# Kernel tuning notes

Hardware: AMD Instinct MI355X
Metric: run time of the kernel (lower is better)

The kernel has to match this reference:

```python
import jax, jax.numpy as jnp
import numpy as np

PATCH = 14

def setup_inputs() -> dict:
    key = jax.random.key(0)
    k1, k2 = jax.random.split(key)
    frames = jax.random.normal(k1, (3, 256, 224, 224), dtype=jnp.float32)
    # per-frame masked patch indices (frame mode), values in [0, num_patches)
    mask_indices = jax.random.randint(k2, (256, 128), 0, 256, dtype=jnp.int64 if jax.config.read('jax_enable_x64') else jnp.int32)
    return {"frames": frames, "mask_indices": mask_indices}

def reference(frames, mask_indices):
    # frames: [C, T, H, W], H == W; mask_indices: [T, num_masked]
    C, T, H, W = frames.shape
    sidelen = W // PATCH  # 16
    # original: h_idx = idx % sidelen (row of patch grid), w_idx = idx // sidelen (col)
    h_idx = mask_indices % sidelen  # [T, M]
    w_idx = mask_indices // sidelen  # [T, M]
    t_idx = jnp.arange(T)[:, None]  # [T, 1] broadcasts against [T, M]
    mask = jnp.ones((T, sidelen, sidelen), dtype=frames.dtype)
    mask = mask.at[t_idx, h_idx, w_idx].set(0.0)  # zero masked patches
    # expand patch-grid mask to pixel mask [T, H, W]
    mask_full = jnp.repeat(jnp.repeat(mask, PATCH, axis=1), PATCH, axis=2)
    return frames * mask_full[None, :, :, :]
```

## Files before the change

kernel.cpp:

```cpp
#include <hip/hip_runtime.h>


constexpr int T_N    = 256;
constexpr int C_N    = 3;
constexpr int H_N    = 224;
constexpr int W_N    = 224;
constexpr int SIDE   = 16;
constexpr int PATCH  = 14;
constexpr int M_N    = 128;
constexpr int F4_ROW = W_N / 4;
constexpr int F4_BAND = PATCH * F4_ROW;
constexpr int F4_PLANE = H_N * W_N / 4;

__global__ __launch_bounds__(256)
void MaskPatches_74818330296837_kernel(const float4* __restrict__ frames,
                                       const int*    __restrict__ midx,
                                       float4*       __restrict__ out)
{
    __shared__ float mrow[SIDE];

    const int bid = blockIdx.x;
    const int ph  = bid & 15;
    const int ct  = bid >> 4;
    const int t   = ct & 255;

    const int tid = threadIdx.x;

    if (tid < SIDE) mrow[tid] = 1.0f;
    __syncthreads();
    if (tid < M_N) {
        const int idx = midx[t * M_N + tid];
        if ((idx & 15) == ph) mrow[idx >> 4] = 0.0f;
    }
    __syncthreads();

    const long long base = (long long)ct * F4_PLANE + (long long)ph * F4_BAND;

    for (int i = tid; i < F4_BAND; i += 256) {
        const int col4 = i % F4_ROW;
        const int w    = col4 * 4;
        float4 v = frames[base + i];
        v.x *= mrow[(w    ) / PATCH];
        v.y *= mrow[(w + 1) / PATCH];
        v.z *= mrow[(w + 2) / PATCH];
        v.w *= mrow[(w + 3) / PATCH];
        out[base + i] = v;
    }
}

extern "C" void kernel_launch(void* const* d_in, const int* in_sizes, int n_in,
                              void* d_out, int out_size, void* d_ws, size_t ws_size,
                              hipStream_t stream) {
    const float4* frames = (const float4*)d_in[0];
    const int*    midx   = (const int*)d_in[1];
    float4*       out    = (float4*)d_out;

    const int grid = C_N * T_N * SIDE;
    MaskPatches_74818330296837_kernel<<<grid, 256, 0, stream>>>(frames, midx, out);
}
```

Measured before the change: 55.13 us.

## Process all channels per block with nontemporal loads and wave-shuffle mask bits

Each block now covers all three channels of one frame band, so the mask is built once per (t, patch-row) instead of three times. The shared-memory mask and its two __syncthreads are replaced by a per-lane bitmask combined with xor shuffles across the 64-lane wave. All twelve loads are issued up front as nontemporal loads, with nontemporal stores at the end, to raise memory-level parallelism and avoid cache pollution. The cost is higher register use and a third as many blocks.

```diff
diff --git a/kernel.cpp b/kernel.cpp
--- a/kernel.cpp
+++ b/kernel.cpp
@@ -1,60 +1,82 @@
 #include <hip/hip_runtime.h>
 
 
-constexpr int T_N    = 256;
-constexpr int C_N    = 3;
-constexpr int H_N    = 224;
-constexpr int W_N    = 224;
-constexpr int SIDE   = 16;
-constexpr int PATCH  = 14;
-constexpr int M_N    = 128;
-constexpr int F4_ROW = W_N / 4;
+typedef float f32x4 __attribute__((ext_vector_type(4)));
+
+constexpr int T_N     = 256;
+constexpr int H_N     = 224;
+constexpr int W_N     = 224;
+constexpr int SIDE    = 16;
+constexpr int PATCH   = 14;
+constexpr int M_N     = 128;
+constexpr int F4_ROW  = W_N / 4;
 constexpr int F4_BAND = PATCH * F4_ROW;
 constexpr int F4_PLANE = H_N * W_N / 4;
+constexpr long long F4_CHAN = (long long)T_N * F4_PLANE;
 
 __global__ __launch_bounds__(256)
-void MaskPatches_74818330296837_kernel(const float4* __restrict__ frames,
-                                       const int*    __restrict__ midx,
-                                       float4*       __restrict__ out)
+void MaskPatches_74818330296837_kernel(const f32x4* __restrict__ frames,
+                                       const int*   __restrict__ midx,
+                                       f32x4*       __restrict__ out)
 {
-    __shared__ float mrow[SIDE];
+    const int bid  = blockIdx.x;
+    const int ph   = bid & 15;
+    const int t    = bid >> 4;
+    const int tid  = threadIdx.x;
+    const int lane = tid & 63;
 
-    const int bid = blockIdx.x;
-    const int ph  = bid & 15;
-    const int ct  = bid >> 4;
-    const int t   = ct & 255;
+    const int* row = midx + t * M_N;
+    const int i0 = row[lane];
+    const int i1 = row[lane + 64];
 
-    const int tid = threadIdx.x;
+    const long long base0 = (long long)t * F4_PLANE + (long long)ph * F4_BAND;
+    const bool tail = tid < (F4_BAND - 3 * 256);
+    f32x4 v[3][4];
+    #pragma unroll
+    for (int c = 0; c < 3; ++c) {
+        const f32x4* p = frames + base0 + c * F4_CHAN;
+        v[c][0] = __builtin_nontemporal_load(p + tid);
+        v[c][1] = __builtin_nontemporal_load(p + tid + 256);
+        v[c][2] = __builtin_nontemporal_load(p + tid + 512);
+        v[c][3] = tail ? __builtin_nontemporal_load(p + tid + 768)
+                       : (f32x4)(0.f);
+    }
 
-    if (tid < SIDE) mrow[tid] = 1.0f;
-    __syncthreads();
-    if (tid < M_N) {
-        const int idx = midx[t * M_N + tid];
-        if ((idx & 15) == ph) mrow[idx >> 4] = 0.0f;
+    unsigned bits = 0;
+    if ((i0 & 15) == ph) bits |= 1u << (i0 >> 4);
+    if ((i1 & 15) == ph) bits |= 1u << (i1 >> 4);
+    #pragma unroll
+    for (int s = 1; s < 64; s <<= 1)
+        bits |= (unsigned)__shfl_xor((int)bits, s, 64);
+
+    f32x4 m[4];
+    #pragma unroll
+    for (int k = 0; k < 4; ++k) {
+        const unsigned i = (unsigned)(tid + k * 256);
+        const unsigned w = (i % F4_ROW) * 4;
+        #pragma unroll
+        for (int j = 0; j < 4; ++j)
+            m[k][j] = ((bits >> ((w + j) / PATCH)) & 1u) ? 0.0f : 1.0f;
     }
-    __syncthreads();
 
-    const long long base = (long long)ct * F4_PLANE + (long long)ph * F4_BAND;
-
-    for (int i = tid; i < F4_BAND; i += 256) {
-        const int col4 = i % F4_ROW;
-        const int w    = col4 * 4;
-        float4 v = frames[base + i];
-        v.x *= mrow[(w    ) / PATCH];
-        v.y *= mrow[(w + 1) / PATCH];
-        v.z *= mrow[(w + 2) / PATCH];
-        v.w *= mrow[(w + 3) / PATCH];
-        out[base + i] = v;
+    #pragma unroll
+    for (int c = 0; c < 3; ++c) {
+        f32x4* q = out + base0 + c * F4_CHAN;
+        #pragma unroll
+        for (int k = 0; k < 3; ++k)
+            __builtin_nontemporal_store(v[c][k] * m[k], q + tid + k * 256);
+        if (tail)
+            __builtin_nontemporal_store(v[c][3] * m[3], q + tid + 768);
     }
 }
 
 extern "C" void kernel_launch(void* const* d_in, const int* in_sizes, int n_in,
                               void* d_out, int out_size, void* d_ws, size_t ws_size,
                               hipStream_t stream) {
-    const float4* frames = (const float4*)d_in[0];
-    const int*    midx   = (const int*)d_in[1];
-    float4*       out    = (float4*)d_out;
+    const f32x4* frames = (const f32x4*)d_in[0];
+    const int*   midx   = (const int*)d_in[1];
+    f32x4*       out    = (f32x4*)d_out;
 
-    const int grid = C_N * T_N * SIDE;
+    const int grid = T_N * SIDE;
     MaskPatches_74818330296837_kernel<<<grid, 256, 0, stream>>>(frames, midx, out);
 }
```

After: 54.51 us. No clear change (-1.1%).
